# Performance work log

Hardware: AMD Instinct MI355X
Metric: run time of the kernel (lower is better)

## Reference

```python
import jax, jax.numpy as jnp
import numpy as np

N_NODES = 50000
N_EDGES = 800000
IN_CH = 128
H_CH = 128


def setup_inputs() -> dict:
    key = jax.random.key(0)
    ks = jax.random.split(key, 8)
    q = jax.random.normal(ks[0], (N_NODES, IN_CH), dtype=jnp.float32)
    k = jax.random.normal(ks[1], (N_NODES, IN_CH), dtype=jnp.float32)
    v = jax.random.normal(ks[2], (N_NODES, IN_CH), dtype=jnp.float32)
    envelope = jax.random.uniform(ks[3], (N_EDGES,), dtype=jnp.float32)
    edge_index = jax.random.randint(ks[4], (2, N_EDGES), 0, N_NODES, dtype=jnp.int64)
    # torch nn.Linear weights are [out, in]; init ~ U(-1/sqrt(fan_in), 1/sqrt(fan_in))
    s = 1.0 / np.sqrt(IN_CH)
    W_l = jax.random.uniform(ks[5], (H_CH, IN_CH), jnp.float32, -s, s)
    W_r = jax.random.uniform(ks[6], (H_CH, IN_CH), jnp.float32, -s, s)
    sa = 1.0 / np.sqrt(H_CH)
    attn_w = jax.random.uniform(ks[7], (1, H_CH), jnp.float32, -sa, sa)
    return {"q": q, "k": k, "v": v, "envelope": envelope,
            "W_l": W_l, "W_r": W_r, "attn_w": attn_w, "edge_index": edge_index}


def reference(q, k, v, envelope, W_l, W_r, attn_w, edge_index):
    # k, v are accepted but unused, matching the original module.
    N = q.shape[0]
    src = edge_index[0]
    dst = edge_index[1]
    g_l = q @ W_l.T                       # [N, H]
    g_r = q @ W_r.T                       # [N, H]
    g_l_src = g_l[src]                    # [E, H] gather
    g_sum = g_l_src + g_r[dst]            # [E, H]
    e = (jax.nn.silu(g_sum) @ attn_w.T)[:, 0]   # [E]
    e = e + jnp.log(envelope + 1e-7)
    # scatter_softmax over dst groups (numerically stable segment softmax)
    seg_max = jax.ops.segment_max(e, dst, num_segments=N)   # [N]
    ex = jnp.exp(e - seg_max[dst])                           # [E]
    denom = jax.ops.segment_sum(ex, dst, num_segments=N)     # [N]
    attn = ex / denom[dst]                                   # [E]
    out = jax.ops.segment_sum(attn[:, None] * g_l_src, dst, num_segments=N)  # [N, H]
    return out
```

## Files before the change

kernel.cpp:

```cpp
#include <hip/hip_runtime.h>
#include <math.h>

#define N_NODES 50000
#define N_EDGES 800000
#define CH 128
#define CAP 48
#define SCAT_BLOCKS ((N_EDGES + 255) / 256)
#define GEMM_BLOCKS ((N_NODES + 63) / 64)

typedef __attribute__((ext_vector_type(8))) short short8;
typedef __attribute__((ext_vector_type(4))) float f32x4;
union FragU { uint4 u; short8 s; };

__device__ __forceinline__ unsigned pack_bf16(float a, float b) {
    unsigned ua = __float_as_uint(a);
    unsigned ub = __float_as_uint(b);
    ua += 0x7FFFu + ((ua >> 16) & 1u);
    ub += 0x7FFFu + ((ub >> 16) & 1u);
    return (ua >> 16) | (ub & 0xFFFF0000u);
}

__global__ __launch_bounds__(256) void prep_pack_kernel(
    const float* __restrict__ W_l, const float* __restrict__ W_r,
    uint4* __restrict__ Wf4)
{
    int tid = blockIdx.x * 256 + threadIdx.x;
    if (tid >= 2 * 8 * 4 * 64) return;
    int lane  = tid & 63;
    int chunk = (tid >> 6) & 3;
    int tile  = (tid >> 8) & 7;
    int mat   = tid >> 11;
    const float* W = mat ? W_r : W_l;
    int n  = tile * 16 + (lane & 15);
    int k0 = chunk * 32 + (lane >> 4) * 8;
    const float* wp = W + n * CH + k0;
    float4 a = *(const float4*)wp;
    float4 b = *(const float4*)(wp + 4);
    uint4 p;
    p.x = pack_bf16(a.x, a.y);
    p.y = pack_bf16(a.z, a.w);
    p.z = pack_bf16(b.x, b.y);
    p.w = pack_bf16(b.z, b.w);
    Wf4[tid] = p;
}

__global__ __launch_bounds__(256) void fused_scatter_gemm_kernel(
    const int* __restrict__ src, const int* __restrict__ dst,
    const float* __restrict__ env,
    int* __restrict__ counts, unsigned* __restrict__ recs,
    const float* __restrict__ q, const uint4* __restrict__ Wf4,
    unsigned short* __restrict__ g_l16, float* __restrict__ g_r)
{
    const int b = blockIdx.x;
    if (b < SCAT_BLOCKS) {
        int i = b * 256 + threadIdx.x;
        if (i < N_EDGES) {
            int d = dst[i];
            int rank = atomicAdd(&counts[d], 1);
            if (rank < CAP) {
                unsigned ev = __float_as_uint(env[i] + 1e-7f);
                ev += 0x7FFFu + ((ev >> 16) & 1u);
                recs[d * CAP + rank] = (unsigned)src[i] | (ev & 0xFFFF0000u);
            }
        }
    } else {
        const int wv   = threadIdx.x >> 6;
        const int lane = threadIdx.x & 63;
        const int m    = lane & 15;
        const int quad = lane >> 4;
        const int row0 = (b - SCAT_BLOCKS) * 64 + wv * 16;

        int arow = row0 + m;
        if (arow >= N_NODES) arow = N_NODES - 1;
        const float* qr = q + (size_t)arow * CH + quad * 8;

        FragU A[4];
        #pragma unroll
        for (int c = 0; c < 4; ++c) {
            float4 x = *(const float4*)(qr + c * 32);
            float4 y = *(const float4*)(qr + c * 32 + 4);
            A[c].u.x = pack_bf16(x.x, x.y);
            A[c].u.y = pack_bf16(x.z, x.w);
            A[c].u.z = pack_bf16(y.x, y.y);
            A[c].u.w = pack_bf16(y.z, y.w);
        }

        for (int mat = 0; mat < 2; ++mat) {
            for (int tile = 0; tile < 8; ++tile) {
                f32x4 acc = {0.f, 0.f, 0.f, 0.f};
                const uint4* bp = Wf4 + (size_t)((mat * 8 + tile) * 4) * 64 + lane;
                #pragma unroll
                for (int c = 0; c < 4; ++c) {
                    FragU B; B.u = bp[c * 64];
                    acc = __builtin_amdgcn_mfma_f32_16x16x32_bf16(A[c].s, B.s, acc, 0, 0, 0);
                }
                int col = tile * 16 + m;
                #pragma unroll
                for (int r = 0; r < 4; ++r) {
                    int rowg = row0 + quad * 4 + r;
                    if (rowg < N_NODES) {
                        if (mat == 0) {
                            unsigned u = __float_as_uint(acc[r]);
                            u += 0x7FFFu + ((u >> 16) & 1u);
                            g_l16[(size_t)rowg * CH + col] = (unsigned short)(u >> 16);
                        } else {
                            g_r[(size_t)rowg * CH + col] = acc[r];
                        }
                    }
                }
            }
        }
    }
}

__global__ __launch_bounds__(256) void node_attn_kernel(
    const uint4* __restrict__ g_lb4, const float* __restrict__ g_r,
    const float* __restrict__ attn_w,
    const unsigned* __restrict__ recs, const int* __restrict__ counts,
    float* __restrict__ out)
{
    int gid = blockIdx.x * blockDim.x + threadIdx.x;
    int wid = gid >> 6;
    if (wid >= N_NODES) return;
    const int lane = threadIdx.x & 63;
    const int q4 = lane >> 4;
    const int sl = lane & 15;

    const int off = wid * CAP;
    int cnt = counts[wid];
    if (cnt > CAP) cnt = CAP;

    float gr[8], aw[8];
    {
        const float4* grp = (const float4*)(g_r + (size_t)wid * CH + sl * 8);
        float4 a = grp[0], b = grp[1];
        gr[0] = a.x; gr[1] = a.y; gr[2] = a.z; gr[3] = a.w;
        gr[4] = b.x; gr[5] = b.y; gr[6] = b.z; gr[7] = b.w;
        const float4* awp = (const float4*)(attn_w + sl * 8);
        float4 c = awp[0], d = awp[1];
        aw[0] = c.x; aw[1] = c.y; aw[2] = c.z; aw[3] = c.w;
        aw[4] = d.x; aw[5] = d.y; aw[6] = d.z; aw[7] = d.w;
    }

    float l = 0.0f;
    float acc[8] = {0.f, 0.f, 0.f, 0.f, 0.f, 0.f, 0.f, 0.f};

    if (cnt > 0) {
        int ec = min(q4, cnt - 1);
        unsigned rc = recs[off + ec];
        int   s_cur  = rc & 0xFFFFu;
        float ev_cur = __uint_as_float(rc & 0xFFFF0000u);
        uint4 g_cur  = g_lb4[(size_t)s_cur * (CH / 8) + sl];

        for (int j = 0; j < cnt; j += 4) {
            int e = j + q4;
            bool active = (e < cnt);
            int enc = min(e + 4, cnt - 1);
            unsigned rn = recs[off + enc];
            int   s_n  = rn & 0xFFFFu;
            float ev_n = __uint_as_float(rn & 0xFFFF0000u);
            uint4 g_n  = g_lb4[(size_t)s_n * (CH / 8) + sl];

            float gl[8];
            gl[0] = __uint_as_float(g_cur.x << 16);
            gl[1] = __uint_as_float(g_cur.x & 0xFFFF0000u);
            gl[2] = __uint_as_float(g_cur.y << 16);
            gl[3] = __uint_as_float(g_cur.y & 0xFFFF0000u);
            gl[4] = __uint_as_float(g_cur.z << 16);
            gl[5] = __uint_as_float(g_cur.z & 0xFFFF0000u);
            gl[6] = __uint_as_float(g_cur.w << 16);
            gl[7] = __uint_as_float(g_cur.w & 0xFFFF0000u);

            float p = 0.0f;
            #pragma unroll
            for (int c = 0; c < 8; ++c) {
                float h = gl[c] + gr[c];
                float sg = __builtin_amdgcn_rcpf(1.0f + __expf(-h));
                p = fmaf(h * aw[c], sg, p);
            }
            p += __shfl_xor(p, 1, 64);
            p += __shfl_xor(p, 2, 64);
            p += __shfl_xor(p, 4, 64);
            p += __shfl_xor(p, 8, 64);

            float w = __expf(p) * (active ? ev_cur : 0.0f);
            l += w;
            #pragma unroll
            for (int c = 0; c < 8; ++c) acc[c] = fmaf(w, gl[c], acc[c]);

            s_cur = s_n; ev_cur = ev_n; g_cur = g_n;
        }
    }

    #pragma unroll
    for (int o = 16; o <= 32; o <<= 1) {
        l += __shfl_xor(l, o, 64);
        #pragma unroll
        for (int c = 0; c < 8; ++c) acc[c] += __shfl_xor(acc[c], o, 64);
    }

    if (q4 == 0) {
        float inv = (l > 0.0f) ? __builtin_amdgcn_rcpf(l) : 0.0f;
        float4 o0 = {acc[0] * inv, acc[1] * inv, acc[2] * inv, acc[3] * inv};
        float4 o1 = {acc[4] * inv, acc[5] * inv, acc[6] * inv, acc[7] * inv};
        float4* op = (float4*)(out + (size_t)wid * CH + sl * 8);
        op[0] = o0;
        op[1] = o1;
    }
}

extern "C" void kernel_launch(void* const* d_in, const int* in_sizes, int n_in,
                              void* d_out, int out_size, void* d_ws, size_t ws_size,
                              hipStream_t stream)
{
    const float* q      = (const float*)d_in[0];
    const float* env    = (const float*)d_in[3];
    const float* W_l    = (const float*)d_in[4];
    const float* W_r    = (const float*)d_in[5];
    const float* attn_w = (const float*)d_in[6];
    const int*   eidx   = (const int*)d_in[7];
    const int* src = eidx;
    const int* dst = eidx + N_EDGES;
    float* out = (float*)d_out;

    float* ws    = (float*)d_ws;
    unsigned* g_lb = (unsigned*)ws;
    float* g_r   = (float*)(g_lb + (size_t)N_NODES * (CH / 2));
    uint4* Wf4   = (uint4*)(g_r + (size_t)N_NODES * CH);
    unsigned* recs = (unsigned*)(Wf4 + 4096);
    int* counts  = (int*)(recs + (size_t)N_NODES * CAP);

    hipMemsetAsync(counts, 0, N_NODES * sizeof(int), stream);

    prep_pack_kernel<<<16, 256, 0, stream>>>(W_l, W_r, Wf4);

    fused_scatter_gemm_kernel<<<SCAT_BLOCKS + GEMM_BLOCKS, 256, 0, stream>>>(
        src, dst, env, counts, recs, q, Wf4, (unsigned short*)g_lb, g_r);

    int node_wave_blocks = (N_NODES * 64 + 255) / 256;
    node_attn_kernel<<<node_wave_blocks, 256, 0, stream>>>(
        (const uint4*)g_lb, g_r, attn_w, recs, counts, out);
}
```

Measured before the change: 224.2 us.

## Interleave GEMM and scatter blocks, deepen gather prefetch, fold memset into prep

The fused scatter/GEMM kernel now places one GEMM block after every four scatter blocks instead of running all scatter blocks first. The aim is to overlap the atomic-heavy scatter with MFMA work across the device. In the node attention kernel, each wave loads all edge records at once and distributes them with shuffles, and gathers are prefetched three groups ahead instead of one, to hide gather latency. The separate memset is folded into the prep kernel, and the intermediate buffers and output now use nontemporal stores and loads. The deeper prefetch raises register pressure and the shuffle-based record indexing adds complexity.

Measured after the change: 233.6 us. 4.2% more time.

```diff
diff --git a/kernel.cpp b/kernel.cpp
--- a/kernel.cpp
+++ b/kernel.cpp
@@ -7,6 +7,7 @@
 #define CAP 48
 #define SCAT_BLOCKS ((N_EDGES + 255) / 256)
 #define GEMM_BLOCKS ((N_NODES + 63) / 64)
+#define TOTAL_BLOCKS (SCAT_BLOCKS + GEMM_BLOCKS)
 
 typedef __attribute__((ext_vector_type(8))) short short8;
 typedef __attribute__((ext_vector_type(4))) float f32x4;
@@ -22,26 +23,28 @@
 
 __global__ __launch_bounds__(256) void prep_pack_kernel(
     const float* __restrict__ W_l, const float* __restrict__ W_r,
-    uint4* __restrict__ Wf4)
+    uint4* __restrict__ Wf4, int* __restrict__ counts)
 {
     int tid = blockIdx.x * 256 + threadIdx.x;
-    if (tid >= 2 * 8 * 4 * 64) return;
-    int lane  = tid & 63;
-    int chunk = (tid >> 6) & 3;
-    int tile  = (tid >> 8) & 7;
-    int mat   = tid >> 11;
-    const float* W = mat ? W_r : W_l;
-    int n  = tile * 16 + (lane & 15);
-    int k0 = chunk * 32 + (lane >> 4) * 8;
-    const float* wp = W + n * CH + k0;
-    float4 a = *(const float4*)wp;
-    float4 b = *(const float4*)(wp + 4);
-    uint4 p;
-    p.x = pack_bf16(a.x, a.y);
-    p.y = pack_bf16(a.z, a.w);
-    p.z = pack_bf16(b.x, b.y);
-    p.w = pack_bf16(b.z, b.w);
-    Wf4[tid] = p;
+    if (tid < 2 * 8 * 4 * 64) {
+        int lane  = tid & 63;
+        int chunk = (tid >> 6) & 3;
+        int tile  = (tid >> 8) & 7;
+        int mat   = tid >> 11;
+        const float* W = mat ? W_r : W_l;
+        int n  = tile * 16 + (lane & 15);
+        int k0 = chunk * 32 + (lane >> 4) * 8;
+        const float* wp = W + n * CH + k0;
+        float4 a = *(const float4*)wp;
+        float4 b = *(const float4*)(wp + 4);
+        uint4 p;
+        p.x = pack_bf16(a.x, a.y);
+        p.y = pack_bf16(a.z, a.w);
+        p.z = pack_bf16(b.x, b.y);
+        p.w = pack_bf16(b.z, b.w);
+        Wf4[tid] = p;
+    }
+    for (int i = tid; i < N_NODES; i += 64 * 256) counts[i] = 0;
 }
 
 __global__ __launch_bounds__(256) void fused_scatter_gemm_kernel(
@@ -52,23 +55,27 @@
     unsigned short* __restrict__ g_l16, float* __restrict__ g_r)
 {
     const int b = blockIdx.x;
-    if (b < SCAT_BLOCKS) {
-        int i = b * 256 + threadIdx.x;
+    const bool is_gemm = ((b % 5) == 0) && (b / 5 < GEMM_BLOCKS);
+    if (!is_gemm) {
+        const int s = b - b / 5 - 1;
+        int i = s * 256 + threadIdx.x;
         if (i < N_EDGES) {
             int d = dst[i];
             int rank = atomicAdd(&counts[d], 1);
             if (rank < CAP) {
                 unsigned ev = __float_as_uint(env[i] + 1e-7f);
                 ev += 0x7FFFu + ((ev >> 16) & 1u);
-                recs[d * CAP + rank] = (unsigned)src[i] | (ev & 0xFFFF0000u);
+                unsigned rec = (unsigned)src[i] | (ev & 0xFFFF0000u);
+                __builtin_nontemporal_store(rec, &recs[d * CAP + rank]);
             }
         }
     } else {
+        const int g    = b / 5;
         const int wv   = threadIdx.x >> 6;
         const int lane = threadIdx.x & 63;
         const int m    = lane & 15;
         const int quad = lane >> 4;
-        const int row0 = (b - SCAT_BLOCKS) * 64 + wv * 16;
+        const int row0 = g * 64 + wv * 16;
 
         int arow = row0 + m;
         if (arow >= N_NODES) arow = N_NODES - 1;
@@ -104,7 +111,7 @@
                             u += 0x7FFFu + ((u >> 16) & 1u);
                             g_l16[(size_t)rowg * CH + col] = (unsigned short)(u >> 16);
                         } else {
-                            g_r[(size_t)rowg * CH + col] = acc[r];
+                            __builtin_nontemporal_store(acc[r], &g_r[(size_t)rowg * CH + col]);
                         }
                     }
                 }
@@ -126,14 +133,14 @@
     const int q4 = lane >> 4;
     const int sl = lane & 15;
 
-    const int off = wid * CAP;
     int cnt = counts[wid];
     if (cnt > CAP) cnt = CAP;
 
     float gr[8], aw[8];
     {
-        const float4* grp = (const float4*)(g_r + (size_t)wid * CH + sl * 8);
-        float4 a = grp[0], b = grp[1];
+        const f32x4* grp = (const f32x4*)(g_r + (size_t)wid * CH + sl * 8);
+        f32x4 a = __builtin_nontemporal_load(grp);
+        f32x4 b = __builtin_nontemporal_load(grp + 1);
         gr[0] = a.x; gr[1] = a.y; gr[2] = a.z; gr[3] = a.w;
         gr[4] = b.x; gr[5] = b.y; gr[6] = b.z; gr[7] = b.w;
         const float4* awp = (const float4*)(attn_w + sl * 8);
@@ -146,30 +153,39 @@
     float acc[8] = {0.f, 0.f, 0.f, 0.f, 0.f, 0.f, 0.f, 0.f};
 
     if (cnt > 0) {
-        int ec = min(q4, cnt - 1);
-        unsigned rc = recs[off + ec];
-        int   s_cur  = rc & 0xFFFFu;
-        float ev_cur = __uint_as_float(rc & 0xFFFF0000u);
-        uint4 g_cur  = g_lb4[(size_t)s_cur * (CH / 8) + sl];
-
-        for (int j = 0; j < cnt; j += 4) {
-            int e = j + q4;
-            bool active = (e < cnt);
-            int enc = min(e + 4, cnt - 1);
-            unsigned rn = recs[off + enc];
-            int   s_n  = rn & 0xFFFFu;
-            float ev_n = __uint_as_float(rn & 0xFFFF0000u);
-            uint4 g_n  = g_lb4[(size_t)s_n * (CH / 8) + sl];
+        const int clampi = cnt - 1;
+        unsigned rcl = recs[wid * CAP + min(lane, clampi)];
+        const int G = (cnt + 3) >> 2;
+
+        #define REC_OF(jg, rv) { int e_ = (jg) * 4 + q4; if (e_ > clampi) e_ = clampi; \
+                                 rv = __shfl(rcl, e_, 64); }
+
+        unsigned r0, r1, r2, r3;
+        uint4 gA, gB, gC, gD;
+        REC_OF(0, r0); gA = g_lb4[(size_t)(r0 & 0xFFFFu) * (CH / 8) + sl];
+        r1 = r0; r2 = r0; gB = gA; gC = gA;
+        if (G > 1) { REC_OF(1, r1); gB = g_lb4[(size_t)(r1 & 0xFFFFu) * (CH / 8) + sl]; }
+        if (G > 2) { REC_OF(2, r2); gC = g_lb4[(size_t)(r2 & 0xFFFFu) * (CH / 8) + sl]; }
+
+        for (int j = 0; j < G; ++j) {
+            r3 = r0; gD = gA;
+            if (j + 3 < G) {
+                REC_OF(j + 3, r3);
+                gD = g_lb4[(size_t)(r3 & 0xFFFFu) * (CH / 8) + sl];
+            }
+
+            bool active = (j * 4 + q4) < cnt;
+            float ev = __uint_as_float(r0 & 0xFFFF0000u);
 
             float gl[8];
-            gl[0] = __uint_as_float(g_cur.x << 16);
-            gl[1] = __uint_as_float(g_cur.x & 0xFFFF0000u);
-            gl[2] = __uint_as_float(g_cur.y << 16);
-            gl[3] = __uint_as_float(g_cur.y & 0xFFFF0000u);
-            gl[4] = __uint_as_float(g_cur.z << 16);
-            gl[5] = __uint_as_float(g_cur.z & 0xFFFF0000u);
-            gl[6] = __uint_as_float(g_cur.w << 16);
-            gl[7] = __uint_as_float(g_cur.w & 0xFFFF0000u);
+            gl[0] = __uint_as_float(gA.x << 16);
+            gl[1] = __uint_as_float(gA.x & 0xFFFF0000u);
+            gl[2] = __uint_as_float(gA.y << 16);
+            gl[3] = __uint_as_float(gA.y & 0xFFFF0000u);
+            gl[4] = __uint_as_float(gA.z << 16);
+            gl[5] = __uint_as_float(gA.z & 0xFFFF0000u);
+            gl[6] = __uint_as_float(gA.w << 16);
+            gl[7] = __uint_as_float(gA.w & 0xFFFF0000u);
 
             float p = 0.0f;
             #pragma unroll
@@ -183,13 +199,14 @@
             p += __shfl_xor(p, 4, 64);
             p += __shfl_xor(p, 8, 64);
 
-            float w = __expf(p) * (active ? ev_cur : 0.0f);
+            float w = __expf(p) * (active ? ev : 0.0f);
             l += w;
             #pragma unroll
             for (int c = 0; c < 8; ++c) acc[c] = fmaf(w, gl[c], acc[c]);
 
-            s_cur = s_n; ev_cur = ev_n; g_cur = g_n;
-        }
+            r0 = r1; gA = gB; r1 = r2; gB = gC; r2 = r3; gC = gD;
+        }
+        #undef REC_OF
     }
 
     #pragma unroll
@@ -201,11 +218,11 @@
 
     if (q4 == 0) {
         float inv = (l > 0.0f) ? __builtin_amdgcn_rcpf(l) : 0.0f;
-        float4 o0 = {acc[0] * inv, acc[1] * inv, acc[2] * inv, acc[3] * inv};
-        float4 o1 = {acc[4] * inv, acc[5] * inv, acc[6] * inv, acc[7] * inv};
-        float4* op = (float4*)(out + (size_t)wid * CH + sl * 8);
-        op[0] = o0;
-        op[1] = o1;
+        f32x4 o0 = {acc[0] * inv, acc[1] * inv, acc[2] * inv, acc[3] * inv};
+        f32x4 o1 = {acc[4] * inv, acc[5] * inv, acc[6] * inv, acc[7] * inv};
+        f32x4* op = (f32x4*)(out + (size_t)wid * CH + sl * 8);
+        __builtin_nontemporal_store(o0, op);
+        __builtin_nontemporal_store(o1, op + 1);
     }
 }
 
@@ -230,11 +247,9 @@
     unsigned* recs = (unsigned*)(Wf4 + 4096);
     int* counts  = (int*)(recs + (size_t)N_NODES * CAP);
 
-    hipMemsetAsync(counts, 0, N_NODES * sizeof(int), stream);
-
-    prep_pack_kernel<<<16, 256, 0, stream>>>(W_l, W_r, Wf4);
-
-    fused_scatter_gemm_kernel<<<SCAT_BLOCKS + GEMM_BLOCKS, 256, 0, stream>>>(
+    prep_pack_kernel<<<64, 256, 0, stream>>>(W_l, W_r, Wf4, counts);
+
+    fused_scatter_gemm_kernel<<<TOTAL_BLOCKS, 256, 0, stream>>>(
         src, dst, env, counts, recs, q, Wf4, (unsigned short*)g_lb, g_r);
 
     int node_wave_blocks = (N_NODES * 64 + 255) / 256;
```
